# Kernel optimization log

Measured on AMD Instinct MI355X. Metric: run time of the kernel, lower is better.

The kernel has to match this reference:

```python
import jax, jax.numpy as jnp
import numpy as np

IN_F, HID, OUT_F, N_HEADS, BATCH = 256, 512, 2048, 8, 4096


def _kaiming_uniform(key, shape, fan_in):
    # kaiming_uniform_ with a=sqrt(5): gain = sqrt(2/(1+5)) = 1/sqrt(3)
    gain = 1.0 / np.sqrt(3.0)
    bound = gain * np.sqrt(3.0 / fan_in)  # = sqrt(1/fan_in)
    return jax.random.uniform(key, shape, jnp.float32, -bound, bound)


def setup_inputs() -> dict:
    key = jax.random.key(0)
    kx, ki, k1, k2, k3, k4 = jax.random.split(key, 6)
    X = jax.random.normal(kx, (BATCH, IN_F), jnp.float32)
    X_head_idx = jax.random.randint(ki, (BATCH,), 0, N_HEADS)
    # layer 1: in -> hidden
    W1 = _kaiming_uniform(k1, (N_HEADS, IN_F, HID), IN_F)
    b1 = jax.random.uniform(k2, (N_HEADS, HID), jnp.float32,
                            -1.0 / np.sqrt(IN_F), 1.0 / np.sqrt(IN_F))
    # layer 2: hidden -> out
    W2 = _kaiming_uniform(k3, (N_HEADS, HID, OUT_F), HID)
    b2 = jax.random.uniform(k4, (N_HEADS, OUT_F), jnp.float32,
                            -1.0 / np.sqrt(HID), 1.0 / np.sqrt(HID))
    return {"X": X, "X_head_idx": X_head_idx, "W1": W1, "b1": b1,
            "W2": W2, "b2": b2}


def _selective_linear(x, idx, W, b):
    # x: [B, in], W: [H, in, out], b: [H, out], idx: [B]
    # compute all heads densely, then select each sample's head
    y = jnp.einsum('bi,hio->bho', x, W) + b[None]   # [B, H, out]
    return jnp.take_along_axis(y, idx[:, None, None], axis=1)[:, 0, :]


def reference(X, X_head_idx, W1, b1, W2, b2):
    h = _selective_linear(X, X_head_idx, W1, b1)
    h = jax.nn.relu(h)
    out = _selective_linear(h, X_head_idx, W2, b2)
    return out
```

## Files before the change

### kernel.cpp

```cpp
#include <hip/hip_runtime.h>

#define IN_F 256
#define HID 512
#define OUT_F 2048
#define N_HEADS 8
#define BATCH 4096

typedef __bf16 bf16_t;
typedef bf16_t bf16x8 __attribute__((ext_vector_type(8)));
typedef float f32x4 __attribute__((ext_vector_type(4)));
typedef unsigned short ushort8 __attribute__((ext_vector_type(8)));

typedef __attribute__((address_space(1))) const unsigned int gu32;
typedef __attribute__((address_space(3))) unsigned int lu32;

__device__ inline unsigned short f2bf(float f) {
  union { float f; unsigned u; } v; v.f = f;
  unsigned u = v.u;
  unsigned r = (u + 0x7FFFu + ((u >> 16) & 1u)) >> 16;
  return (unsigned short)r;
}

__device__ inline void transpose64(const float* __restrict__ W,
                                   unsigned short* __restrict__ Wt,
                                   int K, int N, int b, int nt, int kt,
                                   float (*tile)[65]) {
  int per_head = nt * kt;
  int h = b / per_head;
  int rem = b % per_head;
  int n0 = (rem % nt) * 64;
  int k0 = (rem / nt) * 64;
  const float* Wh = W + (size_t)h * K * N;
  unsigned short* Wth = Wt + (size_t)h * K * N;
  int c = threadIdx.x & 63;
  int r0 = threadIdx.x >> 6;
#pragma unroll
  for (int rr = r0; rr < 64; rr += 4)
    tile[rr][c] = Wh[(size_t)(k0 + rr) * N + n0 + c];
  __syncthreads();
  int c4 = threadIdx.x & 15;
  int r1 = threadIdx.x >> 4;
#pragma unroll
  for (int rr = r1; rr < 64; rr += 16) {
    ushort4 o;
    o.x = f2bf(tile[c4 * 4 + 0][rr]);
    o.y = f2bf(tile[c4 * 4 + 1][rr]);
    o.z = f2bf(tile[c4 * 4 + 2][rr]);
    o.w = f2bf(tile[c4 * 4 + 3][rr]);
    *(ushort4*)&Wth[(size_t)(n0 + rr) * K + k0 + c4 * 4] = o;
  }
}

__global__ __launch_bounds__(256) void k1_kernel(const int* __restrict__ idx,
                                                 int* __restrict__ order,
                                                 int* __restrict__ offsets,
                                                 const float* __restrict__ W1,
                                                 unsigned short* __restrict__ W1t) {
  __shared__ float tile[64][65];
  __shared__ int cnt[N_HEADS];
  __shared__ int base[N_HEADS + 1];
  __shared__ int cur[N_HEADS];
  int b = blockIdx.x;
  if (b == 0) {
    int tid = threadIdx.x;
    if (tid < N_HEADS) cnt[tid] = 0;
    __syncthreads();
    const int4* idx4 = (const int4*)idx;
    int4 v[4];
#pragma unroll
    for (int i = 0; i < 4; ++i) v[i] = idx4[tid + i * 256];
#pragma unroll
    for (int i = 0; i < 4; ++i) {
      atomicAdd(&cnt[v[i].x], 1); atomicAdd(&cnt[v[i].y], 1);
      atomicAdd(&cnt[v[i].z], 1); atomicAdd(&cnt[v[i].w], 1);
    }
    __syncthreads();
    if (tid == 0) {
      int acc = 0;
      for (int h = 0; h < N_HEADS; ++h) { base[h] = acc; cur[h] = acc; acc += cnt[h]; }
      base[N_HEADS] = acc;
    }
    __syncthreads();
    if (tid < N_HEADS + 1) offsets[tid] = base[tid];
#pragma unroll
    for (int i = 0; i < 4; ++i) {
      int i0 = (tid + i * 256) * 4;
      order[atomicAdd(&cur[v[i].x], 1)] = i0;
      order[atomicAdd(&cur[v[i].y], 1)] = i0 + 1;
      order[atomicAdd(&cur[v[i].z], 1)] = i0 + 2;
      order[atomicAdd(&cur[v[i].w], 1)] = i0 + 3;
    }
  } else {
    transpose64(W1, W1t, IN_F, HID, b - 1, HID / 64, IN_F / 64, tile);
  }
}

__device__ inline bool resolve_head(const int* __restrict__ offsets, int my,
                                    int& head, int& row0, int& rows) {
  head = -1; row0 = 0; rows = 0;
  int acc_t = 0;
#pragma unroll
  for (int h = 0; h < N_HEADS; ++h) {
    int o0 = offsets[h], o1 = offsets[h + 1];
    int cnt = o1 - o0;
    int t = (cnt + 127) / 128;
    if (head < 0 && my < acc_t + t) {
      head = h;
      int lt = my - acc_t;
      row0 = o0 + lt * 128;
      rows = min(128, cnt - lt * 128);
    }
    acc_t += t;
  }
  return head >= 0;
}

__device__ void gemm1_body(const float* __restrict__ Xf,
                           const unsigned short* __restrict__ Wt,
                           const float* __restrict__ bias,
                           const int* __restrict__ offsets,
                           const int* __restrict__ order,
                           unsigned short* __restrict__ Hout,
                           unsigned short* As, unsigned short* Bs,
                           int bx, int my) {
  constexpr int K = IN_F, NTOT = HID, BK = 64, NT = K / BK;
  int head, row0, rows;
  if (!resolve_head(offsets, my, head, row0, rows)) return;
  int n0 = bx * 128;
  const unsigned short* Bh = Wt + (size_t)head * (size_t)NTOT * K;

  int tid = threadIdx.x;
  int wave = tid >> 6;
  int lane = tid & 63;
  int q = lane >> 4;
  int l16 = lane & 15;
  int w_m = wave >> 1, w_n = wave & 1;

  int srow = lane >> 3;
  int seg = lane & 7;
  int segl = seg ^ srow;

  const unsigned short* bptr[4];
  const float* gptr[4];
#pragma unroll
  for (int i = 0; i < 4; ++i) {
    int rl = wave * 32 + i * 8 + srow;
    bptr[i] = Bh + (size_t)(n0 + rl) * K + segl * 8;
    int pr = row0 + min(rl, rows - 1);
    gptr[i] = Xf + (size_t)order[pr] * K + segl * 8;
  }

  f32x4 acc[4][4];
#pragma unroll
  for (int i = 0; i < 4; ++i)
#pragma unroll
    for (int j = 0; j < 4; ++j) acc[i][j] = (f32x4){0.f, 0.f, 0.f, 0.f};

#pragma unroll
  for (int t = 0; t < NT; ++t) {
#pragma unroll
    for (int i = 0; i < 4; ++i) {
      __builtin_amdgcn_global_load_lds((gu32*)bptr[i], (lu32*)(Bs + wave * 2048 + i * 512), 16, 0, 0);
      bptr[i] += BK;
    }
#pragma unroll
    for (int i = 0; i < 4; ++i) {
      float4 v0 = *(const float4*)(gptr[i]);
      float4 v1 = *(const float4*)(gptr[i] + 4);
      gptr[i] += BK;
      ushort8 o;
      o[0] = f2bf(v0.x); o[1] = f2bf(v0.y); o[2] = f2bf(v0.z); o[3] = f2bf(v0.w);
      o[4] = f2bf(v1.x); o[5] = f2bf(v1.y); o[6] = f2bf(v1.z); o[7] = f2bf(v1.w);
      int rl = wave * 32 + i * 8 + srow;
      *(ushort8*)(As + rl * 64 + seg * 8) = o;
    }
    __syncthreads();
#pragma unroll
    for (int kk = 0; kk < 2; ++kk) {
      bf16x8 af[4], bfr[4];
#pragma unroll
      for (int i = 0; i < 4; ++i) {
        int ps = ((kk * 4 + q) ^ (l16 & 7)) * 8;
        af[i] = *(const bf16x8*)(As + (w_m * 64 + i * 16 + l16) * 64 + ps);
        bfr[i] = *(const bf16x8*)(Bs + (w_n * 64 + i * 16 + l16) * 64 + ps);
      }
#pragma unroll
      for (int mi = 0; mi < 4; ++mi)
#pragma unroll
        for (int ni = 0; ni < 4; ++ni)
          acc[mi][ni] = __builtin_amdgcn_mfma_f32_16x16x32_bf16(af[mi], bfr[ni], acc[mi][ni], 0, 0, 0);
    }
    __syncthreads();
  }

  float bval[4];
#pragma unroll
  for (int ni = 0; ni < 4; ++ni)
    bval[ni] = bias[(size_t)head * NTOT + n0 + w_n * 64 + ni * 16 + l16];

#pragma unroll
  for (int mi = 0; mi < 4; ++mi) {
#pragma unroll
    for (int r = 0; r < 4; ++r) {
      int m = w_m * 64 + mi * 16 + q * 4 + r;
      if (m < rows) {
        int p = row0 + m;
#pragma unroll
        for (int ni = 0; ni < 4; ++ni) {
          int n = n0 + w_n * 64 + ni * 16 + l16;
          float v = acc[mi][ni][r] + bval[ni];
          v = v > 0.f ? v : 0.f;
          Hout[(size_t)p * NTOT + n] = f2bf(v);
        }
      }
    }
  }
}

__global__ __launch_bounds__(256) void k2_kernel(const float* __restrict__ X,
                                                 const int* __restrict__ order,
                                                 const int* __restrict__ offsets,
                                                 const unsigned short* __restrict__ W1t,
                                                 const float* __restrict__ b1,
                                                 unsigned short* __restrict__ Hb,
                                                 const float* __restrict__ W2,
                                                 unsigned short* __restrict__ W2t) {
  __shared__ __align__(16) unsigned char smem[32768];
  int b = blockIdx.x;
  if (b < 160) {
    gemm1_body(X, W1t, b1, offsets, order, Hb,
               (unsigned short*)smem, (unsigned short*)(smem + 16384),
               b & 3, b >> 2);
  } else {
    transpose64(W2, W2t, HID, OUT_F, b - 160, OUT_F / 64, HID / 64,
                (float(*)[65])smem);
  }
}

__global__ __launch_bounds__(256) void gemm2_kernel(const unsigned short* __restrict__ A,
                                                    const unsigned short* __restrict__ Wt,
                                                    const float* __restrict__ bias,
                                                    const int* __restrict__ offsets,
                                                    const int* __restrict__ order,
                                                    float* __restrict__ Out) {
  constexpr int K = HID, NTOT = OUT_F, BK = 64, NT = K / BK;
  __shared__ __align__(16) unsigned short As[2][128 * BK];
  __shared__ __align__(16) unsigned short Bs[2][128 * BK];

  int head, row0, rows;
  if (!resolve_head(offsets, blockIdx.y, head, row0, rows)) return;
  int n0 = blockIdx.x * 128;
  const unsigned short* Bh = Wt + (size_t)head * (size_t)NTOT * K;

  int tid = threadIdx.x;
  int wave = tid >> 6;
  int lane = tid & 63;
  int q = lane >> 4;
  int l16 = lane & 15;
  int w_m = wave >> 1, w_n = wave & 1;

  int srow = lane >> 3;
  int seg = lane & 7;
  int segl = seg ^ srow;

  const unsigned short* aptr[4];
  const unsigned short* bptr[4];
#pragma unroll
  for (int i = 0; i < 4; ++i) {
    int rl = wave * 32 + i * 8 + srow;
    bptr[i] = Bh + (size_t)(n0 + rl) * K + segl * 8;
    int pr = row0 + min(rl, rows - 1);
    aptr[i] = A + (size_t)pr * K + segl * 8;
  }

  f32x4 acc[4][4];
#pragma unroll
  for (int i = 0; i < 4; ++i)
#pragma unroll
    for (int j = 0; j < 4; ++j) acc[i][j] = (f32x4){0.f, 0.f, 0.f, 0.f};

#pragma unroll
  for (int i = 0; i < 4; ++i) {
    __builtin_amdgcn_global_load_lds((gu32*)bptr[i], (lu32*)(&Bs[0][wave * 2048 + i * 512]), 16, 0, 0);
    bptr[i] += BK;
    __builtin_amdgcn_global_load_lds((gu32*)aptr[i], (lu32*)(&As[0][wave * 2048 + i * 512]), 16, 0, 0);
    aptr[i] += BK;
  }
  __syncthreads();

  int cur = 0;
#pragma unroll
  for (int t = 0; t < NT; ++t) {
    if (t + 1 < NT) {
#pragma unroll
      for (int i = 0; i < 4; ++i) {
        __builtin_amdgcn_global_load_lds((gu32*)bptr[i], (lu32*)(&Bs[cur ^ 1][wave * 2048 + i * 512]), 16, 0, 0);
        bptr[i] += BK;
        __builtin_amdgcn_global_load_lds((gu32*)aptr[i], (lu32*)(&As[cur ^ 1][wave * 2048 + i * 512]), 16, 0, 0);
        aptr[i] += BK;
      }
    }
#pragma unroll
    for (int kk = 0; kk < 2; ++kk) {
      bf16x8 af[4], bfr[4];
#pragma unroll
      for (int i = 0; i < 4; ++i) {
        int ps = ((kk * 4 + q) ^ (l16 & 7)) * 8;
        af[i] = *(const bf16x8*)(&As[cur][(w_m * 64 + i * 16 + l16) * 64 + ps]);
        bfr[i] = *(const bf16x8*)(&Bs[cur][(w_n * 64 + i * 16 + l16) * 64 + ps]);
      }
#pragma unroll
      for (int mi = 0; mi < 4; ++mi)
#pragma unroll
        for (int ni = 0; ni < 4; ++ni)
          acc[mi][ni] = __builtin_amdgcn_mfma_f32_16x16x32_bf16(af[mi], bfr[ni], acc[mi][ni], 0, 0, 0);
    }
    __syncthreads();
    cur ^= 1;
  }

  float bval[4];
#pragma unroll
  for (int ni = 0; ni < 4; ++ni)
    bval[ni] = bias[(size_t)head * NTOT + n0 + w_n * 64 + ni * 16 + l16];

#pragma unroll
  for (int mi = 0; mi < 4; ++mi) {
#pragma unroll
    for (int r = 0; r < 4; ++r) {
      int m = w_m * 64 + mi * 16 + q * 4 + r;
      if (m < rows) {
        int rg = order[row0 + m];
#pragma unroll
        for (int ni = 0; ni < 4; ++ni) {
          int n = n0 + w_n * 64 + ni * 16 + l16;
          Out[(size_t)rg * NTOT + n] = acc[mi][ni][r] + bval[ni];
        }
      }
    }
  }
}

extern "C" void kernel_launch(void* const* d_in, const int* in_sizes, int n_in,
                              void* d_out, int out_size, void* d_ws, size_t ws_size,
                              hipStream_t stream) {
  const float* X = (const float*)d_in[0];
  const int* idxh = (const int*)d_in[1];
  const float* W1 = (const float*)d_in[2];
  const float* b1 = (const float*)d_in[3];
  const float* W2 = (const float*)d_in[4];
  const float* b2 = (const float*)d_in[5];
  float* out = (float*)d_out;

  char* ws = (char*)d_ws;
  int* order = (int*)ws;                     ws += (size_t)BATCH * 4;
  int* offsets = (int*)ws;                   ws += 64;
  unsigned short* W1t = (unsigned short*)ws; ws += (size_t)N_HEADS * IN_F * HID * 2;
  unsigned short* W2t = (unsigned short*)ws; ws += (size_t)N_HEADS * HID * OUT_F * 2;
  unsigned short* Hb = (unsigned short*)ws;  ws += (size_t)BATCH * HID * 2;

  k1_kernel<<<dim3(257), dim3(256), 0, stream>>>(idxh, order, offsets, W1, W1t);
  k2_kernel<<<dim3(2208), dim3(256), 0, stream>>>(X, order, offsets, W1t, b1, Hb, W2, W2t);

  constexpr int MT = BATCH / 128 + N_HEADS;
  gemm2_kernel<<<dim3(OUT_F / 128, MT), dim3(256), 0, stream>>>(
      Hb, W2t, b2, offsets, order, out);
}
```

Measured before the change: 138.8 us.

## Pre-convert X to bf16 and load gemm1 A tiles via direct-to-LDS loads

Adds a bf16 conversion pass over X in the first kernel, using 128 extra blocks, so gemm1 can stream A rows with global_load_lds instead of loading fp32, converting and storing to LDS in registers. The transpose tile loads are also widened to float4. This moves conversion work off the GEMM critical loop and halves the A-operand bytes gemm1 reads. In exchange it adds an extra write and read of a 2 MB buffer and more blocks in the first launch.

```diff
diff --git a/kernel.cpp b/kernel.cpp
--- a/kernel.cpp
+++ b/kernel.cpp
@@ -9,7 +9,6 @@
 typedef __bf16 bf16_t;
 typedef bf16_t bf16x8 __attribute__((ext_vector_type(8)));
 typedef float f32x4 __attribute__((ext_vector_type(4)));
-typedef unsigned short ushort8 __attribute__((ext_vector_type(8)));
 
 typedef __attribute__((address_space(1))) const unsigned int gu32;
 typedef __attribute__((address_space(3))) unsigned int lu32;
@@ -32,11 +31,16 @@
   int k0 = (rem / nt) * 64;
   const float* Wh = W + (size_t)h * K * N;
   unsigned short* Wth = Wt + (size_t)h * K * N;
-  int c = threadIdx.x & 63;
-  int r0 = threadIdx.x >> 6;
-#pragma unroll
-  for (int rr = r0; rr < 64; rr += 4)
-    tile[rr][c] = Wh[(size_t)(k0 + rr) * N + n0 + c];
+  int c16 = threadIdx.x & 15;
+  int r16 = threadIdx.x >> 4;
+#pragma unroll
+  for (int rr = r16; rr < 64; rr += 16) {
+    float4 v = *(const float4*)&Wh[(size_t)(k0 + rr) * N + n0 + c16 * 4];
+    tile[rr][c16 * 4 + 0] = v.x;
+    tile[rr][c16 * 4 + 1] = v.y;
+    tile[rr][c16 * 4 + 2] = v.z;
+    tile[rr][c16 * 4 + 3] = v.w;
+  }
   __syncthreads();
   int c4 = threadIdx.x & 15;
   int r1 = threadIdx.x >> 4;
@@ -52,6 +56,8 @@
 }
 
 __global__ __launch_bounds__(256) void k1_kernel(const int* __restrict__ idx,
+                                                 const float* __restrict__ X,
+                                                 unsigned short* __restrict__ Xb,
                                                  int* __restrict__ order,
                                                  int* __restrict__ offsets,
                                                  const float* __restrict__ W1,
@@ -61,8 +67,8 @@
   __shared__ int base[N_HEADS + 1];
   __shared__ int cur[N_HEADS];
   int b = blockIdx.x;
+  int tid = threadIdx.x;
   if (b == 0) {
-    int tid = threadIdx.x;
     if (tid < N_HEADS) cnt[tid] = 0;
     __syncthreads();
     const int4* idx4 = (const int4*)idx;
@@ -90,8 +96,19 @@
       order[atomicAdd(&cur[v[i].z], 1)] = i0 + 2;
       order[atomicAdd(&cur[v[i].w], 1)] = i0 + 3;
     }
+  } else if (b < 129) {
+    const float4* X4 = (const float4*)X;
+    ushort4* O4 = (ushort4*)Xb;
+    int base_i = (b - 1) * 2048 + tid;
+#pragma unroll
+    for (int it = 0; it < 8; ++it) {
+      float4 v = X4[base_i + it * 256];
+      ushort4 o;
+      o.x = f2bf(v.x); o.y = f2bf(v.y); o.z = f2bf(v.z); o.w = f2bf(v.w);
+      O4[base_i + it * 256] = o;
+    }
   } else {
-    transpose64(W1, W1t, IN_F, HID, b - 1, HID / 64, IN_F / 64, tile);
+    transpose64(W1, W1t, IN_F, HID, b - 129, HID / 64, IN_F / 64, tile);
   }
 }
 
@@ -115,7 +132,7 @@
   return head >= 0;
 }
 
-__device__ void gemm1_body(const float* __restrict__ Xf,
+__device__ void gemm1_body(const unsigned short* __restrict__ Xb,
                            const unsigned short* __restrict__ Wt,
                            const float* __restrict__ bias,
                            const int* __restrict__ offsets,
@@ -140,14 +157,14 @@
   int seg = lane & 7;
   int segl = seg ^ srow;
 
+  const unsigned short* aptr[4];
   const unsigned short* bptr[4];
-  const float* gptr[4];
 #pragma unroll
   for (int i = 0; i < 4; ++i) {
     int rl = wave * 32 + i * 8 + srow;
     bptr[i] = Bh + (size_t)(n0 + rl) * K + segl * 8;
     int pr = row0 + min(rl, rows - 1);
-    gptr[i] = Xf + (size_t)order[pr] * K + segl * 8;
+    aptr[i] = Xb + (size_t)order[pr] * K + segl * 8;
   }
 
   f32x4 acc[4][4];
@@ -162,17 +179,8 @@
     for (int i = 0; i < 4; ++i) {
       __builtin_amdgcn_global_load_lds((gu32*)bptr[i], (lu32*)(Bs + wave * 2048 + i * 512), 16, 0, 0);
       bptr[i] += BK;
-    }
-#pragma unroll
-    for (int i = 0; i < 4; ++i) {
-      float4 v0 = *(const float4*)(gptr[i]);
-      float4 v1 = *(const float4*)(gptr[i] + 4);
-      gptr[i] += BK;
-      ushort8 o;
-      o[0] = f2bf(v0.x); o[1] = f2bf(v0.y); o[2] = f2bf(v0.z); o[3] = f2bf(v0.w);
-      o[4] = f2bf(v1.x); o[5] = f2bf(v1.y); o[6] = f2bf(v1.z); o[7] = f2bf(v1.w);
-      int rl = wave * 32 + i * 8 + srow;
-      *(ushort8*)(As + rl * 64 + seg * 8) = o;
+      __builtin_amdgcn_global_load_lds((gu32*)aptr[i], (lu32*)(As + wave * 2048 + i * 512), 16, 0, 0);
+      aptr[i] += BK;
     }
     __syncthreads();
 #pragma unroll
@@ -217,7 +225,7 @@
   }
 }
 
-__global__ __launch_bounds__(256) void k2_kernel(const float* __restrict__ X,
+__global__ __launch_bounds__(256) void k2_kernel(const unsigned short* __restrict__ Xb,
                                                  const int* __restrict__ order,
                                                  const int* __restrict__ offsets,
                                                  const unsigned short* __restrict__ W1t,
@@ -228,7 +236,7 @@
   __shared__ __align__(16) unsigned char smem[32768];
   int b = blockIdx.x;
   if (b < 160) {
-    gemm1_body(X, W1t, b1, offsets, order, Hb,
+    gemm1_body(Xb, W1t, b1, offsets, order, Hb,
                (unsigned short*)smem, (unsigned short*)(smem + 16384),
                b & 3, b >> 2);
   } else {
@@ -355,12 +363,13 @@
   char* ws = (char*)d_ws;
   int* order = (int*)ws;                     ws += (size_t)BATCH * 4;
   int* offsets = (int*)ws;                   ws += 64;
+  unsigned short* Xb = (unsigned short*)ws;  ws += (size_t)BATCH * IN_F * 2;
   unsigned short* W1t = (unsigned short*)ws; ws += (size_t)N_HEADS * IN_F * HID * 2;
   unsigned short* W2t = (unsigned short*)ws; ws += (size_t)N_HEADS * HID * OUT_F * 2;
   unsigned short* Hb = (unsigned short*)ws;  ws += (size_t)BATCH * HID * 2;
 
-  k1_kernel<<<dim3(257), dim3(256), 0, stream>>>(idxh, order, offsets, W1, W1t);
-  k2_kernel<<<dim3(2208), dim3(256), 0, stream>>>(X, order, offsets, W1t, b1, Hb, W2, W2t);
+  k1_kernel<<<dim3(385), dim3(256), 0, stream>>>(idxh, X, Xb, order, offsets, W1, W1t);
+  k2_kernel<<<dim3(2208), dim3(256), 0, stream>>>(Xb, order, offsets, W1t, b1, Hb, W2, W2t);
 
   constexpr int MT = BATCH / 128 + N_HEADS;
   gemm2_kernel<<<dim3(OUT_F / 128, MT), dim3(256), 0, stream>>>(
```

Result: faster. 132.6 us (-4.5%).
